# Performance work log

Measured on AMD Instinct MI355X. Metric: run time of the kernel, lower is better.

## Reference

```python
import jax, jax.numpy as jnp
import numpy as np

N, IC, H, W = 4, 64, 256, 256
GROUPS, KS = 8, 3
OC = 64


def setup_inputs() -> dict:
    key = jax.random.key(0)
    k1, k2 = jax.random.split(key)
    x = jax.random.normal(k1, (N, IC, H, W), dtype=jnp.float32)
    w = jax.random.normal(k2, (N, GROUPS, KS * KS, H, W), dtype=jnp.float32)
    return {"x": x, "w": w, "out_channels": OC}


def reference(x, w, out_channels):
    # x: [n, ic, H, W]; w: [n, groups, ks*ks, H, W]
    n, ic, h, wid = x.shape
    groups = w.shape[1]
    ks = int(round(float(np.sqrt(w.shape[2]))))
    pad = (ks - 1) // 2
    group_in = ic // groups
    group_out = out_channels // groups
    # Per-pixel weight is shared across output channels of a group and
    # multiplies the sum over the group's input channels.
    xs = x.reshape(n, groups, group_in, h, wid).sum(axis=2)  # [n, g, H, W]
    xp = jnp.pad(xs, ((0, 0), (0, 0), (pad, pad), (pad, pad)))
    og = jnp.zeros((n, groups, h, wid), dtype=x.dtype)
    for kh in range(ks):
        for kw in range(ks):
            og = og + w[:, :, kh * ks + kw] * xp[:, :, kh:kh + h, kw:kw + wid]
    # broadcast group output to group_out consecutive channels
    o = jnp.repeat(og, group_out, axis=1)  # [n, out_channels, H, W]
    return o
```

## Files before the change

### kernel.cpp

```cpp
#include <hip/hip_runtime.h>

#define NB 4
#define IC 64
#define HH 256
#define WW 256
#define GROUPS 8
#define GROUP_IN 8
#define GROUP_OUT 8

constexpr int HW = HH * WW;
constexpr int PLANES = NB * GROUPS;
constexpr int VEC4_PER_PLANE = HW / 4;
constexpr int TOTAL_VEC4 = PLANES * VEC4_PER_PLANE;

__global__ __launch_bounds__(256) void ska_group_sum(const float* __restrict__ x,
                                                     float* __restrict__ xs) {
    int gid = blockIdx.x * 256 + threadIdx.x;
    if (gid >= TOTAL_VEC4) return;
    int plane  = gid >> 14;
    int within = gid & 16383;
    const float4* xp = reinterpret_cast<const float4*>(x)
                     + (size_t)plane * GROUP_IN * VEC4_PER_PLANE + within;
    float4 acc = xp[0];
#pragma unroll
    for (int c = 1; c < GROUP_IN; ++c) {
        float4 v = xp[(size_t)c * VEC4_PER_PLANE];
        acc.x += v.x; acc.y += v.y; acc.z += v.z; acc.w += v.w;
    }
    reinterpret_cast<float4*>(xs)[(size_t)plane * VEC4_PER_PLANE + within] = acc;
}

__global__ __launch_bounds__(256) void ska_conv(const float* __restrict__ wgt,
                                                const float* __restrict__ xs,
                                                float* __restrict__ out) {
    int gid = blockIdx.x * 256 + threadIdx.x;
    if (gid >= TOTAL_VEC4) return;
    int plane  = gid >> 14;
    int within = gid & 16383;
    int y  = within >> 6;
    int x0 = (within & 63) << 2;

    const float* xsp = xs + (size_t)plane * HW;

    float e[3][6];
#pragma unroll
    for (int r = 0; r < 3; ++r) {
        int yy = y + r - 1;
        if (yy < 0 || yy >= HH) {
#pragma unroll
            for (int j = 0; j < 6; ++j) e[r][j] = 0.f;
        } else {
            const float* rp = xsp + (size_t)yy * WW;
            float4 v = *reinterpret_cast<const float4*>(rp + x0);
            e[r][1] = v.x; e[r][2] = v.y; e[r][3] = v.z; e[r][4] = v.w;
            e[r][0] = (x0 > 0)       ? rp[x0 - 1] : 0.f;
            e[r][5] = (x0 + 4 < WW)  ? rp[x0 + 4] : 0.f;
        }
    }

    const float* wbase = wgt + (size_t)plane * 9 * HW + (size_t)y * WW + x0;
    float4 acc = {0.f, 0.f, 0.f, 0.f};
#pragma unroll
    for (int kh = 0; kh < 3; ++kh) {
#pragma unroll
        for (int kw = 0; kw < 3; ++kw) {
            float4 wv = *reinterpret_cast<const float4*>(wbase + (size_t)(kh * 3 + kw) * HW);
            acc.x += wv.x * e[kh][kw + 0];
            acc.y += wv.y * e[kh][kw + 1];
            acc.z += wv.z * e[kh][kw + 2];
            acc.w += wv.w * e[kh][kw + 3];
        }
    }

    int n = plane >> 3;
    int g = plane & 7;
    float4* ob = reinterpret_cast<float4*>(out)
               + ((size_t)(n * IC + g * GROUP_OUT) * VEC4_PER_PLANE)
               + ((size_t)y * WW + x0) / 4;
#pragma unroll
    for (int j = 0; j < GROUP_OUT; ++j) ob[(size_t)j * VEC4_PER_PLANE] = acc;
}

extern "C" void kernel_launch(void* const* d_in, const int* in_sizes, int n_in,
                              void* d_out, int out_size, void* d_ws, size_t ws_size,
                              hipStream_t stream) {
    const float* x   = (const float*)d_in[0];
    const float* wgt = (const float*)d_in[1];
    float* out = (float*)d_out;
    float* xs  = (float*)d_ws;

    constexpr int THREADS = 256;
    constexpr int BLOCKS  = (TOTAL_VEC4 + THREADS - 1) / THREADS;

    ska_group_sum<<<BLOCKS, THREADS, 0, stream>>>(x, xs);
    ska_conv<<<BLOCKS, THREADS, 0, stream>>>(wgt, xs, out);
}
```

Before: 40.36 us.

## Fuse group-sum and per-pixel conv into one kernel with shared-memory halo tiles

Merges the channel group-sum kernel and the 3x3 per-pixel-weight conv into a single kernel. Each block computes the group-summed input for a 16-row tile plus halo rows into shared memory, then runs the conv from LDS. This removes the global intermediate write and read and one launch. In exchange it re-reads halo rows of x and uses fewer, larger blocks with a barrier, which may reduce latency hiding.

```diff
diff --git a/kernel.cpp b/kernel.cpp
--- a/kernel.cpp
+++ b/kernel.cpp
@@ -1,84 +1,90 @@
 #include <hip/hip_runtime.h>
 
 #define NB 4
-#define IC 64
+#define ICC 64
 #define HH 256
 #define WW 256
-#define GROUPS 8
 #define GROUP_IN 8
 #define GROUP_OUT 8
+#define TROWS 16
+#define HALO_ROWS (TROWS + 2)
 
 constexpr int HW = HH * WW;
-constexpr int PLANES = NB * GROUPS;
-constexpr int VEC4_PER_PLANE = HW / 4;
-constexpr int TOTAL_VEC4 = PLANES * VEC4_PER_PLANE;
+constexpr int PLANES = NB * 8;
+constexpr int TILES_PER_PLANE = HH / TROWS;
+constexpr int W4 = WW / 4;
+constexpr int THREADS = 512;
 
-__global__ __launch_bounds__(256) void ska_group_sum(const float* __restrict__ x,
-                                                     float* __restrict__ xs) {
-    int gid = blockIdx.x * 256 + threadIdx.x;
-    if (gid >= TOTAL_VEC4) return;
-    int plane  = gid >> 14;
-    int within = gid & 16383;
-    const float4* xp = reinterpret_cast<const float4*>(x)
-                     + (size_t)plane * GROUP_IN * VEC4_PER_PLANE + within;
-    float4 acc = xp[0];
+__global__ __launch_bounds__(THREADS) void ska_fused(const float* __restrict__ x,
+                                                     const float* __restrict__ wgt,
+                                                     float* __restrict__ out) {
+    __shared__ float xs[HALO_ROWS][WW];
+
+    const int bid   = blockIdx.x;
+    const int plane = bid >> 4;
+    const int tile  = bid & 15;
+    const int y0    = tile * TROWS;
+    const int tid   = threadIdx.x;
+
+    const float4* xbase = reinterpret_cast<const float4*>(x)
+                        + (size_t)plane * GROUP_IN * (HW / 4);
+    for (int idx = tid; idx < HALO_ROWS * W4; idx += THREADS) {
+        const int r  = idx >> 6;
+        const int c4 = idx & 63;
+        const int yy = y0 - 1 + r;
+        float4 acc = {0.f, 0.f, 0.f, 0.f};
+        if (yy >= 0 && yy < HH) {
+            const float4* p = xbase + (size_t)yy * W4 + c4;
 #pragma unroll
-    for (int c = 1; c < GROUP_IN; ++c) {
-        float4 v = xp[(size_t)c * VEC4_PER_PLANE];
-        acc.x += v.x; acc.y += v.y; acc.z += v.z; acc.w += v.w;
+            for (int c = 0; c < GROUP_IN; ++c) {
+                float4 v = p[(size_t)c * (HW / 4)];
+                acc.x += v.x; acc.y += v.y; acc.z += v.z; acc.w += v.w;
+            }
+        }
+        *reinterpret_cast<float4*>(&xs[r][c4 * 4]) = acc;
     }
-    reinterpret_cast<float4*>(xs)[(size_t)plane * VEC4_PER_PLANE + within] = acc;
-}
+    __syncthreads();
 
-__global__ __launch_bounds__(256) void ska_conv(const float* __restrict__ wgt,
-                                                const float* __restrict__ xs,
-                                                float* __restrict__ out) {
-    int gid = blockIdx.x * 256 + threadIdx.x;
-    if (gid >= TOTAL_VEC4) return;
-    int plane  = gid >> 14;
-    int within = gid & 16383;
-    int y  = within >> 6;
-    int x0 = (within & 63) << 2;
+    const int c4    = tid & 63;
+    const int x0    = c4 * 4;
+    const int rbase = tid >> 6;
+    const float* wplane = wgt + (size_t)plane * 9 * HW;
+    const int n = plane >> 3, g = plane & 7;
+    float4* outbase = reinterpret_cast<float4*>(out)
+                    + (size_t)(n * ICC + g * GROUP_OUT) * (HW / 4);
 
-    const float* xsp = xs + (size_t)plane * HW;
+#pragma unroll
+    for (int s = 0; s < 2; ++s) {
+        const int lr = s * 8 + rbase;
+        const int y  = y0 + lr;
 
-    float e[3][6];
+        float e[3][6];
 #pragma unroll
-    for (int r = 0; r < 3; ++r) {
-        int yy = y + r - 1;
-        if (yy < 0 || yy >= HH) {
-#pragma unroll
-            for (int j = 0; j < 6; ++j) e[r][j] = 0.f;
-        } else {
-            const float* rp = xsp + (size_t)yy * WW;
+        for (int r = 0; r < 3; ++r) {
+            const float* rp = &xs[lr + r][0];
             float4 v = *reinterpret_cast<const float4*>(rp + x0);
             e[r][1] = v.x; e[r][2] = v.y; e[r][3] = v.z; e[r][4] = v.w;
-            e[r][0] = (x0 > 0)       ? rp[x0 - 1] : 0.f;
-            e[r][5] = (x0 + 4 < WW)  ? rp[x0 + 4] : 0.f;
+            e[r][0] = (x0 > 0)      ? rp[x0 - 1] : 0.f;
+            e[r][5] = (x0 + 4 < WW) ? rp[x0 + 4] : 0.f;
         }
+
+        const float* wb = wplane + (size_t)y * WW + x0;
+        float4 acc = {0.f, 0.f, 0.f, 0.f};
+#pragma unroll
+        for (int kh = 0; kh < 3; ++kh)
+#pragma unroll
+            for (int kw = 0; kw < 3; ++kw) {
+                float4 wv = *reinterpret_cast<const float4*>(wb + (size_t)(kh * 3 + kw) * HW);
+                acc.x += wv.x * e[kh][kw + 0];
+                acc.y += wv.y * e[kh][kw + 1];
+                acc.z += wv.z * e[kh][kw + 2];
+                acc.w += wv.w * e[kh][kw + 3];
+            }
+
+        float4* ob = outbase + ((size_t)y * WW + x0) / 4;
+#pragma unroll
+        for (int j = 0; j < GROUP_OUT; ++j) ob[(size_t)j * (HW / 4)] = acc;
     }
-
-    const float* wbase = wgt + (size_t)plane * 9 * HW + (size_t)y * WW + x0;
-    float4 acc = {0.f, 0.f, 0.f, 0.f};
-#pragma unroll
-    for (int kh = 0; kh < 3; ++kh) {
-#pragma unroll
-        for (int kw = 0; kw < 3; ++kw) {
-            float4 wv = *reinterpret_cast<const float4*>(wbase + (size_t)(kh * 3 + kw) * HW);
-            acc.x += wv.x * e[kh][kw + 0];
-            acc.y += wv.y * e[kh][kw + 1];
-            acc.z += wv.z * e[kh][kw + 2];
-            acc.w += wv.w * e[kh][kw + 3];
-        }
-    }
-
-    int n = plane >> 3;
-    int g = plane & 7;
-    float4* ob = reinterpret_cast<float4*>(out)
-               + ((size_t)(n * IC + g * GROUP_OUT) * VEC4_PER_PLANE)
-               + ((size_t)y * WW + x0) / 4;
-#pragma unroll
-    for (int j = 0; j < GROUP_OUT; ++j) ob[(size_t)j * VEC4_PER_PLANE] = acc;
 }
 
 extern "C" void kernel_launch(void* const* d_in, const int* in_sizes, int n_in,
@@ -87,11 +93,7 @@
     const float* x   = (const float*)d_in[0];
     const float* wgt = (const float*)d_in[1];
     float* out = (float*)d_out;
-    float* xs  = (float*)d_ws;
 
-    constexpr int THREADS = 256;
-    constexpr int BLOCKS  = (TOTAL_VEC4 + THREADS - 1) / THREADS;
-
-    ska_group_sum<<<BLOCKS, THREADS, 0, stream>>>(x, xs);
-    ska_conv<<<BLOCKS, THREADS, 0, stream>>>(wgt, xs, out);
+    constexpr int BLOCKS = PLANES * TILES_PER_PLANE;
+    ska_fused<<<BLOCKS, THREADS, 0, stream>>>(x, wgt, out);
 }
```

New measurement: 36.40 us. 9.8% less time.
